# Optimization experiments

Measured on AMD Instinct MI355X. Metric: run time of the kernel, lower is better.

## Reference

```python
import jax, jax.numpy as jnp
import numpy as np

B, N, C, H, E = 16, 512, 128, 8, 131072
Nn = B * N
Dh = C // H
EPS = 1e-5


def setup_inputs() -> dict:
    key = jax.random.key(0)
    ks = jax.random.split(key, 16)
    s = C ** -0.5
    x = jax.random.normal(ks[0], (Nn, C), dtype=jnp.float32)
    edge_index = jax.random.randint(ks[1], (2, E), 0, Nn)
    batch = jnp.arange(Nn) // N  # B equal-sized graphs, sorted
    attn_bias = jax.random.normal(ks[2], (B, N, N, H), dtype=jnp.float32)
    return {
        "x": x,
        "edge_index": edge_index,
        "batch": batch,
        "attn_bias": attn_bias,
        "conv_w": jax.random.normal(ks[3], (C, C)) * s,
        "conv_b": jnp.zeros((C,)),
        "wq": jax.random.normal(ks[4], (C, C)) * s,
        "bq": jnp.zeros((C,)),
        "wk": jax.random.normal(ks[5], (C, C)) * s,
        "bk": jnp.zeros((C,)),
        "wv": jax.random.normal(ks[6], (C, C)) * s,
        "bv": jnp.zeros((C,)),
        "wo": jax.random.normal(ks[7], (C, C)) * s,
        "bo": jnp.zeros((C,)),
        "w1": jax.random.normal(ks[8], (C, 2 * C)) * s,
        "b1": jnp.zeros((2 * C,)),
        "w2": jax.random.normal(ks[9], (2 * C, C)) * (2 * C) ** -0.5,
        "b2": jnp.zeros((C,)),
        "g1": jnp.ones((C,)), "be1": jnp.zeros((C,)),
        "g2": jnp.ones((C,)), "be2": jnp.zeros((C,)),
        "g3": jnp.ones((C,)), "be3": jnp.zeros((C,)),
    }


def _bn(h, g, b):
    # BatchNorm1d over the node dimension (training-mode batch statistics)
    mu = h.mean(axis=0)
    var = h.var(axis=0)  # biased, matches torch normalization
    return g * (h - mu) * jax.lax.rsqrt(var + EPS) + b


def reference(x, edge_index, batch, attn_bias,
              conv_w, conv_b, wq, bq, wk, bk, wv, bv, wo, bo,
              w1, b1, w2, b2, g1, be1, g2, be2, g3, be3):
    n_nodes, ch = x.shape
    bsz, n_max, _, heads = attn_bias.shape
    dh = ch // heads

    # ---- GCN conv (self loops + symmetric norm) -> dropout(0) + residual + norm1
    loops = jnp.arange(n_nodes)
    src = jnp.concatenate([edge_index[0], loops])
    dst = jnp.concatenate([edge_index[1], loops])
    deg = jax.ops.segment_sum(jnp.ones_like(src, dtype=x.dtype), dst, num_segments=n_nodes)
    dinv = jax.lax.rsqrt(jnp.maximum(deg, 1.0))
    xw = x @ conv_w
    msg = xw[src] * (dinv[src] * dinv[dst])[:, None]
    hconv = jax.ops.segment_sum(msg, dst, num_segments=n_nodes) + conv_b
    h1 = _bn(hconv + x, g1, be1)

    # ---- dense batch (equal-sized sorted graphs -> pure reshape, mask all-valid)
    xd = x.reshape(bsz, n_max, ch)
    q = ((xd @ wq + bq) * (dh ** -0.5)).reshape(bsz, n_max, heads, dh)
    k = (xd @ wk + bk).reshape(bsz, n_max, heads, dh)
    v = (xd @ wv + bv).reshape(bsz, n_max, heads, dh)
    scores = jnp.einsum('bqhd,bkhd->bqkh', q, k) + attn_bias  # [B,N,N,H]
    probs = jax.nn.softmax(scores, axis=2)
    att = jnp.einsum('bqkh,bkhd->bqhd', probs, v).reshape(bsz, n_max, ch)
    att = att @ wo + bo
    h2 = _bn(att.reshape(n_nodes, ch) + x, g2, be2)

    # ---- combine branches, MLP with residual, norm3
    out = h1 + h2
    mlp = jax.nn.relu(out @ w1 + b1) @ w2 + b2
    return _bn(out + mlp, g3, be3)
```

## Files before the change

### kernel.cpp

```cpp
#include <hip/hip_runtime.h>
#include <cstddef>

#define NN 8192
#define CC 128

typedef unsigned short u16;
typedef _Float16 half_t;
typedef _Float16 v4h __attribute__((ext_vector_type(4)));
typedef float v4f __attribute__((ext_vector_type(4)));

static __device__ inline u16 f2bf1(float x) {
  unsigned u = __builtin_bit_cast(unsigned, x);
  u += 0x7fffu + ((u >> 16) & 1u);
  return (u16)(u >> 16);
}
static __device__ inline float bf_lo(unsigned u) { return __builtin_bit_cast(float, u << 16); }
static __device__ inline float bf_hi(unsigned u) { return __builtin_bit_cast(float, u & 0xffff0000u); }

typedef __attribute__((address_space(3))) void lvoid_t;
static __device__ inline unsigned lds_addr(void* p) {
  return (unsigned)(unsigned long long)(lvoid_t*)p;
}


__global__ __launch_bounds__(256) void count_deg_int_k(const int* __restrict__ dst, int* degi, int E) {
  int i = blockIdx.x * 256 + threadIdx.x;
  if (i < E) atomicAdd(&degi[dst[i]], 1);
}

__global__ __launch_bounds__(256) void dinv_k(const int* __restrict__ degi, float* __restrict__ dinv, int n) {
  int i = blockIdx.x * 256 + threadIdx.x;
  if (i < n) dinv[i] = rsqrtf((float)(degi[i] + 1));
}

__global__ __launch_bounds__(256) void scan_k(const int* __restrict__ degi, int* __restrict__ rowstart,
                                              int* __restrict__ cursor) {
  __shared__ int partial[256];
  int t = threadIdx.x;
  int base = t * 32;
  int local[32];
  int s = 0;
#pragma unroll
  for (int i = 0; i < 32; ++i) { local[i] = s; s += degi[base + i]; }
  partial[t] = s;
  __syncthreads();
  for (int off = 1; off < 256; off <<= 1) {
    int v = (t >= off) ? partial[t - off] : 0;
    __syncthreads();
    partial[t] += v;
    __syncthreads();
  }
  int offset = partial[t] - s;
#pragma unroll
  for (int i = 0; i < 32; ++i) {
    rowstart[base + i] = offset + local[i];
    cursor[base + i] = offset + local[i];
  }
  if (t == 255) rowstart[NN] = offset + s;
}

__global__ __launch_bounds__(256) void bucket_k(const int* __restrict__ src, const int* __restrict__ dst,
    int* __restrict__ cursor, int* __restrict__ col, int E) {
  int e = blockIdx.x * 256 + threadIdx.x;
  if (e >= E) return;
  int d = dst[e];
  int pos = atomicAdd(&cursor[d], 1);
  col[pos] = src[e];
}

__global__ __launch_bounds__(256) void gather_k(const int* __restrict__ rowstart, const int* __restrict__ col,
    const float* __restrict__ xws, const float* __restrict__ dinv, const float* __restrict__ cb,
    const float* __restrict__ x, float* __restrict__ h1) {
  int d = blockIdx.x * 2 + (threadIdx.x >> 7);
  int c = threadIdx.x & 127;
  int j0 = rowstart[d], j1 = rowstart[d + 1];
  float dd = dinv[d];
  float sum = 0.f;
  float v = 0.f;
  if (j0 < j1) v = xws[(size_t)col[j0] * CC + c];
  for (int j = j0; j < j1; ++j) {
    float v_next = 0.f;
    if (j + 1 < j1) v_next = xws[(size_t)col[j + 1] * CC + c];
    sum += v;
    v = v_next;
  }
  int idx = d * CC + c;
  sum += xws[idx];
  h1[idx] = sum * dd + cb[c] + x[idx];
}


__global__ __launch_bounds__(256) void bn_stats_k(const float* __restrict__ X,
    float* __restrict__ sums, float* __restrict__ sumsq) {
  int t = threadIdx.x;
  int c = t & 127, rg = t >> 7;
  int r0 = blockIdx.x * 64;
  float s = 0.f, sq = 0.f;
  for (int i = 0; i < 32; ++i) {
    float v = X[(size_t)(r0 + rg + 2 * i) * CC + c];
    s += v; sq += v * v;
  }
  atomicAdd(&sums[c], s);
  atomicAdd(&sumsq[c], sq);
}

__global__ __launch_bounds__(256) void combine_k(const float* __restrict__ h1, const float* __restrict__ h2,
    const float* __restrict__ st, const float* __restrict__ g1, const float* __restrict__ be1,
    const float* __restrict__ g2, const float* __restrict__ be2, float* __restrict__ out) {
  int idx = blockIdx.x * 256 + threadIdx.x;
  int c = idx & 127;
  float mu1 = st[c] * (1.f / NN);
  float var1 = st[128 + c] * (1.f / NN) - mu1 * mu1;
  float sc1 = g1[c] * rsqrtf(var1 + 1e-5f);
  float sh1 = be1[c] - mu1 * sc1;
  float mu2 = st[256 + c] * (1.f / NN);
  float var2 = st[384 + c] * (1.f / NN) - mu2 * mu2;
  float sc2 = g2[c] * rsqrtf(var2 + 1e-5f);
  float sh2 = be2[c] - mu2 * sc2;
  out[idx] = sc1 * h1[idx] + sh1 + sc2 * h2[idx] + sh2;
}

__global__ __launch_bounds__(256) void bn_apply_k(const float* __restrict__ h, const float* __restrict__ st,
    const float* __restrict__ g3, const float* __restrict__ be3, float* __restrict__ out) {
  int idx = blockIdx.x * 256 + threadIdx.x;
  int c = idx & 127;
  float mu = st[512 + c] * (1.f / NN);
  float var = st[640 + c] * (1.f / NN) - mu * mu;
  float sc = g3[c] * rsqrtf(var + 1e-5f);
  float sh = be3[c] - mu * sc;
  out[idx] = sc * h[idx] + sh;
}

__global__ __launch_bounds__(256) void gemm_k(const float* __restrict__ A, const float* __restrict__ W,
    const float* __restrict__ bias, const float* __restrict__ resid, const float* __restrict__ dscale,
    float* __restrict__ out, int M, int N, int K, float scale, int relu, int ofp16) {
  __shared__ float As[64 * 132];
  __shared__ float Ws[128 * 64];
  int t = threadIdx.x;
  int ty = t >> 4, tx = t & 15;
  int row0 = blockIdx.x * 64, n0 = blockIdx.y * 64;
  float acc[4][4] = {};
  for (int kc = 0; kc < K; kc += 128) {
#pragma unroll
    for (int j = 0; j < 8; ++j) {
      int f = t + 256 * j;
      int r = f >> 5, c4 = f & 31;
      *(float4*)(As + r * 132 + c4 * 4) = *(const float4*)(A + (size_t)(row0 + r) * K + kc + c4 * 4);
    }
#pragma unroll
    for (int j = 0; j < 8; ++j) {
      int f = t + 256 * j;
      int kr = f >> 4, c4 = f & 15;
      *(float4*)(Ws + kr * 64 + c4 * 4) = *(const float4*)(W + (size_t)(kc + kr) * N + n0 + c4 * 4);
    }
    __syncthreads();
    for (int k0 = 0; k0 < 128; k0 += 4) {
      float a[4][4], b[4][4];
#pragma unroll
      for (int i = 0; i < 4; ++i) {
        float4 t4 = *(const float4*)(As + (4 * ty + i) * 132 + k0);
        a[i][0] = t4.x; a[i][1] = t4.y; a[i][2] = t4.z; a[i][3] = t4.w;
      }
#pragma unroll
      for (int kk = 0; kk < 4; ++kk) {
        float4 t4 = *(const float4*)(Ws + (k0 + kk) * 64 + 4 * tx);
        b[kk][0] = t4.x; b[kk][1] = t4.y; b[kk][2] = t4.z; b[kk][3] = t4.w;
      }
#pragma unroll
      for (int kk = 0; kk < 4; ++kk)
#pragma unroll
        for (int i = 0; i < 4; ++i)
#pragma unroll
          for (int j = 0; j < 4; ++j)
            acc[i][j] += a[i][kk] * b[kk][j];
    }
    __syncthreads();
  }
  float4 bv = make_float4(0.f, 0.f, 0.f, 0.f);
  if (bias) bv = *(const float4*)(bias + n0 + 4 * tx);
#pragma unroll
  for (int i = 0; i < 4; ++i) {
    int row = row0 + 4 * ty + i;
    float ds = dscale ? dscale[row] : 1.f;
    float4 r;
    r.x = (acc[i][0] + bv.x) * scale * ds;
    r.y = (acc[i][1] + bv.y) * scale * ds;
    r.z = (acc[i][2] + bv.z) * scale * ds;
    r.w = (acc[i][3] + bv.w) * scale * ds;
    if (relu) { r.x = fmaxf(r.x, 0.f); r.y = fmaxf(r.y, 0.f); r.z = fmaxf(r.z, 0.f); r.w = fmaxf(r.w, 0.f); }
    size_t o = (size_t)row * N + n0 + 4 * tx;
    if (ofp16) {
      half_t* oh = (half_t*)out;
      v4h hv;
      hv[0] = (half_t)r.x; hv[1] = (half_t)r.y; hv[2] = (half_t)r.z; hv[3] = (half_t)r.w;
      *(v4h*)(oh + o) = hv;
    } else {
      if (resid) {
        float4 rv = *(const float4*)(resid + o);
        r.x += rv.x; r.y += rv.y; r.z += rv.z; r.w += rv.w;
      }
      *(float4*)(out + o) = r;
    }
  }
}

__global__ __launch_bounds__(64, 3) void attn_k(const half_t* __restrict__ Qh,
    const half_t* __restrict__ Kh, const half_t* __restrict__ Vh, const float* __restrict__ bias,
    u16* __restrict__ p0, u16* __restrict__ p1, u16* __restrict__ p2, u16* __restrict__ p3,
    float* __restrict__ lbuf) {
  __shared__ u16 VL[2][2048];
  const int t = threadIdx.x;
  const int orig = blockIdx.x;
  const int s = orig & 7;
  const int qtg = orig >> 3;
  const int b = qtg >> 5;
  const int key0 = s * 64;
  const int node_t = qtg * 16;
  const int kb0 = b * 512 + key0;
  const int lq = t & 15;
  const int lg = t >> 4;

  v4h qf[8];
#pragma unroll
  for (int hd = 0; hd < 8; ++hd)
    qf[hd] = *(const v4h*)(Qh + (size_t)(node_t + lq) * CC + hd * 16 + lg * 4);

  v4f oacc[8];
  float lacc[8];
#pragma unroll
  for (int hd = 0; hd < 8; ++hd) { oacc[hd] = (v4f){0.f, 0.f, 0.f, 0.f}; lacc[hd] = 0.f; }

  const int v_hdb = t >> 5;
  const int v_kg = (t >> 3) & 3;
  const int v_km = (t >> 1) & 3;
  const int v_dm0 = (t & 1) * 8;
  uint4 vreg[4];

  auto vload = [&](int ch) {
#pragma unroll
    for (int i = 0; i < 4; ++i)
      vreg[i] = *(const uint4*)(Vh + (size_t)(kb0 + ch * 16 + v_kg * 4 + v_km) * CC
                                + (i * 2 + v_hdb) * 16 + v_dm0);
  };
  auto vwrite = [&](int bf) {
#pragma unroll
    for (int i = 0; i < 4; ++i)
      *(uint4*)&VL[bf][i * 512 + t * 8] = vreg[i];
  };

  const unsigned lbase = lds_addr(&VL[0][0]);
  const float* bb = bias + ((size_t)node_t * 512 + key0) * 8 + (size_t)lq * 4096;

  vload(0);
  vwrite(0);

  for (int ch = 0; ch < 4; ++ch) {
    const int bf = ch & 1;
    if (ch < 3) vload(ch + 1);

    v4h kf[8];
#pragma unroll
    for (int hd = 0; hd < 8; ++hd)
      kf[hd] = *(const v4h*)(Kh + (size_t)(kb0 + ch * 16 + lq) * CC + hd * 16 + lg * 4);

    asm volatile("s_waitcnt lgkmcnt(0)" ::: "memory");
    __builtin_amdgcn_sched_barrier(0);
    unsigned va = lbase + (unsigned)(bf * 4096) + (unsigned)(t * 8);
    unsigned long long vfr[8];
#pragma unroll
    for (int hd = 0; hd < 8; ++hd)
      asm volatile("ds_read_b64_tr_b16 %0, %1 offset:%2"
                   : "=v"(vfr[hd]) : "v"(va), "i"(hd * 512));
    asm volatile("s_waitcnt lgkmcnt(0)" ::: "memory");
    __builtin_amdgcn_sched_barrier(0);

    if (ch < 3) vwrite(bf ^ 1);

    const v4f z = (v4f){0.f, 0.f, 0.f, 0.f};
#pragma unroll
    for (int hg = 0; hg < 2; ++hg) {
      v4f bfr[4];
#pragma unroll
      for (int reg = 0; reg < 4; ++reg)
        bfr[reg] = *(const v4f*)(bb + (size_t)(ch * 16 + lg * 4 + reg) * 8 + hg * 4);

      v4f stv[4];
#pragma unroll
      for (int j = 0; j < 4; ++j)
        stv[j] = __builtin_amdgcn_mfma_f32_16x16x16f16(kf[hg * 4 + j], qf[hg * 4 + j], z, 0, 0, 0);

#pragma unroll
      for (int j = 0; j < 4; ++j) {
        const int hd = hg * 4 + j;
        float pr0 = __expf(stv[j][0] + bfr[0][j] - 4.f);
        float pr1 = __expf(stv[j][1] + bfr[1][j] - 4.f);
        float pr2 = __expf(stv[j][2] + bfr[2][j] - 4.f);
        float pr3 = __expf(stv[j][3] + bfr[3][j] - 4.f);
        lacc[hd] += pr0 + pr1 + pr2 + pr3;
        unsigned u0 = __builtin_bit_cast(unsigned, __builtin_amdgcn_cvt_pkrtz(pr0, pr1));
        unsigned u1 = __builtin_bit_cast(unsigned, __builtin_amdgcn_cvt_pkrtz(pr2, pr3));
        uint2 pu = make_uint2(u0, u1);
        v4h pa = __builtin_bit_cast(v4h, pu);
        v4h vf = __builtin_bit_cast(v4h, vfr[hd]);
        oacc[hd] = __builtin_amdgcn_mfma_f32_16x16x16f16(pa, vf, oacc[hd], 0, 0, 0);
      }
    }
  }

  u16* preg = (s < 4) ? ((s < 2) ? p0 : p1) : ((s < 6) ? p2 : p3);
  u16* pbase = preg + (size_t)(s & 1) * ((size_t)NN * CC);
#pragma unroll
  for (int hd = 0; hd < 8; ++hd)
#pragma unroll
    for (int reg = 0; reg < 4; ++reg)
      pbase[(((size_t)qtg * 8 + hd) * 4 + reg) * 64 + t] = f2bf1(oacc[hd][reg]);

#pragma unroll
  for (int hd = 0; hd < 8; ++hd) {
    float v = lacc[hd];
    v += __shfl_xor(v, 16);
    v += __shfl_xor(v, 32);
    lacc[hd] = v;
  }
  if (t < 16) {
#pragma unroll
    for (int hd = 0; hd < 8; ++hd)
      lbuf[s * 65536 + (node_t + t) * 8 + hd] = lacc[hd];
  }
}

__global__ __launch_bounds__(256) void attn_merge_k(const u16* __restrict__ p0,
    const u16* __restrict__ p1, const u16* __restrict__ p2, const u16* __restrict__ p3,
    const float* __restrict__ lbuf, float* __restrict__ out) {
  int i = blockIdx.x * 256 + threadIdx.x;
  int node = i >> 3, h = i & 7;
  int tile = node >> 4, q = node & 15;
  float L = 0.f;
#pragma unroll
  for (int s = 0; s < 8; ++s) L += lbuf[s * 65536 + i];
  float inv = 1.f / L;
  float o[16];
#pragma unroll
  for (int d = 0; d < 16; ++d) o[d] = 0.f;
  const u16* regs[4] = {p0, p1, p2, p3};
  size_t base = (((size_t)tile * 8 + h) * 4 + (q & 3)) * 64 + (q >> 2) * 16;
#pragma unroll
  for (int s = 0; s < 8; ++s) {
    const u16* pb = regs[s >> 1] + (size_t)(s & 1) * ((size_t)NN * CC) + base;
    uint4 a = *(const uint4*)pb;
    uint4 b = *(const uint4*)(pb + 8);
    unsigned u[8] = {a.x, a.y, a.z, a.w, b.x, b.y, b.z, b.w};
#pragma unroll
    for (int j = 0; j < 8; ++j) {
      o[2 * j]     += bf_lo(u[j]);
      o[2 * j + 1] += bf_hi(u[j]);
    }
  }
  float* po = out + (size_t)i * 16;
#pragma unroll
  for (int j = 0; j < 4; ++j)
    *(float4*)(po + 4 * j) = make_float4(o[4*j] * inv, o[4*j+1] * inv, o[4*j+2] * inv, o[4*j+3] * inv);
}


extern "C" void kernel_launch(void* const* d_in, const int* in_sizes, int n_in,
                              void* d_out, int out_size, void* d_ws, size_t ws_size,
                              hipStream_t stream) {
  const float* x      = (const float*)d_in[0];
  const int*   ei     = (const int*)d_in[1];
  const float* bias   = (const float*)d_in[3];
  const float* conv_w = (const float*)d_in[4];
  const float* conv_b = (const float*)d_in[5];
  const float* wq = (const float*)d_in[6];
  const float* bq = (const float*)d_in[7];
  const float* wk = (const float*)d_in[8];
  const float* bk = (const float*)d_in[9];
  const float* wv = (const float*)d_in[10];
  const float* bv = (const float*)d_in[11];
  const float* wo = (const float*)d_in[12];
  const float* bo = (const float*)d_in[13];
  const float* w1 = (const float*)d_in[14];
  const float* b1 = (const float*)d_in[15];
  const float* w2 = (const float*)d_in[16];
  const float* b2 = (const float*)d_in[17];
  const float* g1 = (const float*)d_in[18];
  const float* be1 = (const float*)d_in[19];
  const float* g2 = (const float*)d_in[20];
  const float* be2 = (const float*)d_in[21];
  const float* g3 = (const float*)d_in[22];
  const float* be3 = (const float*)d_in[23];
  int E = in_sizes[1] / 2;

  float* ws = (float*)d_ws;
  const size_t NC = (size_t)NN * CC;
  float* xw     = ws;
  float* h1pre  = ws + NC;
  float* qb     = ws + 2 * NC;
  float* kb     = ws + 3 * NC;
  float* vb     = ws + 4 * NC;
  float* h2pre  = ws + 5 * NC;
  float* outbuf = ws + 6 * NC;
  float* hid    = ws + 2 * NC;
  float* h3pre  = ws + 4 * NC;
  float* st     = ws + 7 * NC;
  float* dinv   = ws + 7 * NC + 768;
  int*   degi     = (int*)(ws + 7 * NC + 768 + NN);
  int*   rowstart = degi + NN;
  int*   cursor   = rowstart + NN + 1;
  int*   col      = cursor + NN;
  float* lbuf     = (float*)(col + E);

  hipMemsetAsync(degi, 0, NN * sizeof(int), stream);
  hipMemsetAsync(st, 0, 768 * sizeof(float), stream);

  count_deg_int_k<<<(E + 255) / 256, 256, 0, stream>>>(ei + E, degi, E);
  dinv_k<<<NN / 256, 256, 0, stream>>>(degi, dinv, NN);
  scan_k<<<1, 256, 0, stream>>>(degi, rowstart, cursor);
  bucket_k<<<(E + 255) / 256, 256, 0, stream>>>(ei, ei + E, cursor, col, E);
  gemm_k<<<dim3(NN / 64, 2), 256, 0, stream>>>(x, conv_w, nullptr, nullptr, dinv, xw, NN, CC, CC, 1.f, 0, 0);
  gather_k<<<NN / 2, 256, 0, stream>>>(rowstart, col, xw, dinv, conv_b, x, h1pre);
  bn_stats_k<<<NN / 64, 256, 0, stream>>>(h1pre, st + 0, st + 128);

  gemm_k<<<dim3(NN / 64, 2), 256, 0, stream>>>(x, wq, bq, nullptr, nullptr, qb, NN, CC, CC, 0.25f, 0, 1);
  gemm_k<<<dim3(NN / 64, 2), 256, 0, stream>>>(x, wk, bk, nullptr, nullptr, kb, NN, CC, CC, 1.f, 0, 1);
  gemm_k<<<dim3(NN / 64, 2), 256, 0, stream>>>(x, wv, bv, nullptr, nullptr, vb, NN, CC, CC, 1.f, 0, 1);
  attn_k<<<4096, 64, 0, stream>>>((const half_t*)qb, (const half_t*)kb, (const half_t*)vb, bias,
      (u16*)xw, (u16*)h2pre, (u16*)d_out, (u16*)outbuf, lbuf);
  attn_merge_k<<<65536 / 256, 256, 0, stream>>>((const u16*)xw, (const u16*)h2pre,
      (const u16*)d_out, (const u16*)outbuf, lbuf, vb);
  gemm_k<<<dim3(NN / 64, 2), 256, 0, stream>>>(vb, wo, bo, x, nullptr, h2pre, NN, CC, CC, 1.f, 0, 0);
  bn_stats_k<<<NN / 64, 256, 0, stream>>>(h2pre, st + 256, st + 384);

  combine_k<<<NC / 256, 256, 0, stream>>>(h1pre, h2pre, st, g1, be1, g2, be2, outbuf);
  gemm_k<<<dim3(NN / 64, 4), 256, 0, stream>>>(outbuf, w1, b1, nullptr, nullptr, hid, NN, 2 * CC, CC, 1.f, 1, 0);
  gemm_k<<<dim3(NN / 64, 2), 256, 0, stream>>>(hid, w2, b2, outbuf, nullptr, h3pre, NN, CC, 2 * CC, 1.f, 0, 0);
  bn_stats_k<<<NN / 64, 256, 0, stream>>>(h3pre, st + 512, st + 640);
  bn_apply_k<<<NC / 256, 256, 0, stream>>>(h3pre, st, g3, be3, (float*)d_out);
}
```

Measured before the change: 422.7 us.

## Replace FP32 SIMT GEMM with fp16 MFMA matrix-core GEMM

Swaps the scalar FP32 register-tiled GEMM used for every dense projection (conv, Q/K/V, output, MLP) for an MFMA 16x16x16 fp16 kernel. The weight tile is transposed into LDS as fp16, and A rows are loaded straight from global memory and converted to fp16 in registers. The aim is to move the projection FLOPs off the vector ALUs and onto the matrix cores. The cost is reduced precision on all GEMM inputs (fp16 operands, fp32 accumulation) and narrower, less coalesced scalar output stores.

```diff
diff --git a/kernel.cpp b/kernel.cpp
--- a/kernel.cpp
+++ b/kernel.cpp
@@ -131,75 +131,64 @@
   out[idx] = sc * h[idx] + sh;
 }
 
-__global__ __launch_bounds__(256) void gemm_k(const float* __restrict__ A, const float* __restrict__ W,
+template <int KT>
+__global__ __launch_bounds__(256) void mgemm_k(const float* __restrict__ A, const float* __restrict__ W,
     const float* __restrict__ bias, const float* __restrict__ resid, const float* __restrict__ dscale,
-    float* __restrict__ out, int M, int N, int K, float scale, int relu, int ofp16) {
-  __shared__ float As[64 * 132];
-  __shared__ float Ws[128 * 64];
-  int t = threadIdx.x;
-  int ty = t >> 4, tx = t & 15;
-  int row0 = blockIdx.x * 64, n0 = blockIdx.y * 64;
-  float acc[4][4] = {};
-  for (int kc = 0; kc < K; kc += 128) {
-#pragma unroll
-    for (int j = 0; j < 8; ++j) {
-      int f = t + 256 * j;
-      int r = f >> 5, c4 = f & 31;
-      *(float4*)(As + r * 132 + c4 * 4) = *(const float4*)(A + (size_t)(row0 + r) * K + kc + c4 * 4);
+    float* __restrict__ out, int N, float scale, int relu, int ofp16) {
+  __shared__ half_t Wt[64][KT + 8];
+  const int t = threadIdx.x;
+  const int row0 = blockIdx.x * 64, n0 = blockIdx.y * 64;
+
+#pragma unroll
+  for (int i = 0; i < KT / 4; ++i) {
+    int idx = t + 256 * i;
+    int n = idx & 63, k = idx >> 6;
+    Wt[n][k] = (half_t)W[(size_t)k * N + n0 + n];
+  }
+  __syncthreads();
+
+  const int wv = t >> 6, lg = (t >> 4) & 3, lq = t & 15;
+  const int arow = row0 + wv * 16 + lq;
+
+  v4f af[KT / 16];
+#pragma unroll
+  for (int i = 0; i < KT / 16; ++i)
+    af[i] = *(const v4f*)(A + (size_t)arow * KT + i * 16 + lg * 4);
+
+  v4f acc[4];
+#pragma unroll
+  for (int c = 0; c < 4; ++c) acc[c] = (v4f){0.f, 0.f, 0.f, 0.f};
+
+#pragma unroll
+  for (int i = 0; i < KT / 16; ++i) {
+    v4h a;
+    a[0] = (half_t)af[i][0]; a[1] = (half_t)af[i][1];
+    a[2] = (half_t)af[i][2]; a[3] = (half_t)af[i][3];
+#pragma unroll
+    for (int c = 0; c < 4; ++c) {
+      v4h b = *(const v4h*)&Wt[c * 16 + lq][i * 16 + lg * 4];
+      acc[c] = __builtin_amdgcn_mfma_f32_16x16x16f16(a, b, acc[c], 0, 0, 0);
     }
-#pragma unroll
-    for (int j = 0; j < 8; ++j) {
-      int f = t + 256 * j;
-      int kr = f >> 4, c4 = f & 15;
-      *(float4*)(Ws + kr * 64 + c4 * 4) = *(const float4*)(W + (size_t)(kc + kr) * N + n0 + c4 * 4);
-    }
-    __syncthreads();
-    for (int k0 = 0; k0 < 128; k0 += 4) {
-      float a[4][4], b[4][4];
-#pragma unroll
-      for (int i = 0; i < 4; ++i) {
-        float4 t4 = *(const float4*)(As + (4 * ty + i) * 132 + k0);
-        a[i][0] = t4.x; a[i][1] = t4.y; a[i][2] = t4.z; a[i][3] = t4.w;
+  }
+
+  float bc[4];
+#pragma unroll
+  for (int c = 0; c < 4; ++c) bc[c] = bias ? bias[n0 + c * 16 + lq] : 0.f;
+#pragma unroll
+  for (int reg = 0; reg < 4; ++reg) {
+    int row = row0 + wv * 16 + lg * 4 + reg;
+    float ds = dscale ? dscale[row] : 1.f;
+#pragma unroll
+    for (int c = 0; c < 4; ++c) {
+      float r = (acc[c][reg] + bc[c]) * scale * ds;
+      if (relu) r = fmaxf(r, 0.f);
+      size_t o = (size_t)row * N + n0 + c * 16 + lq;
+      if (ofp16) {
+        ((half_t*)out)[o] = (half_t)r;
+      } else {
+        if (resid) r += resid[o];
+        out[o] = r;
       }
-#pragma unroll
-      for (int kk = 0; kk < 4; ++kk) {
-        float4 t4 = *(const float4*)(Ws + (k0 + kk) * 64 + 4 * tx);
-        b[kk][0] = t4.x; b[kk][1] = t4.y; b[kk][2] = t4.z; b[kk][3] = t4.w;
-      }
-#pragma unroll
-      for (int kk = 0; kk < 4; ++kk)
-#pragma unroll
-        for (int i = 0; i < 4; ++i)
-#pragma unroll
-          for (int j = 0; j < 4; ++j)
-            acc[i][j] += a[i][kk] * b[kk][j];
-    }
-    __syncthreads();
-  }
-  float4 bv = make_float4(0.f, 0.f, 0.f, 0.f);
-  if (bias) bv = *(const float4*)(bias + n0 + 4 * tx);
-#pragma unroll
-  for (int i = 0; i < 4; ++i) {
-    int row = row0 + 4 * ty + i;
-    float ds = dscale ? dscale[row] : 1.f;
-    float4 r;
-    r.x = (acc[i][0] + bv.x) * scale * ds;
-    r.y = (acc[i][1] + bv.y) * scale * ds;
-    r.z = (acc[i][2] + bv.z) * scale * ds;
-    r.w = (acc[i][3] + bv.w) * scale * ds;
-    if (relu) { r.x = fmaxf(r.x, 0.f); r.y = fmaxf(r.y, 0.f); r.z = fmaxf(r.z, 0.f); r.w = fmaxf(r.w, 0.f); }
-    size_t o = (size_t)row * N + n0 + 4 * tx;
-    if (ofp16) {
-      half_t* oh = (half_t*)out;
-      v4h hv;
-      hv[0] = (half_t)r.x; hv[1] = (half_t)r.y; hv[2] = (half_t)r.z; hv[3] = (half_t)r.w;
-      *(v4h*)(oh + o) = hv;
-    } else {
-      if (resid) {
-        float4 rv = *(const float4*)(resid + o);
-        r.x += rv.x; r.y += rv.y; r.z += rv.z; r.w += rv.w;
-      }
-      *(float4*)(out + o) = r;
     }
   }
 }
@@ -417,23 +406,23 @@
   dinv_k<<<NN / 256, 256, 0, stream>>>(degi, dinv, NN);
   scan_k<<<1, 256, 0, stream>>>(degi, rowstart, cursor);
   bucket_k<<<(E + 255) / 256, 256, 0, stream>>>(ei, ei + E, cursor, col, E);
-  gemm_k<<<dim3(NN / 64, 2), 256, 0, stream>>>(x, conv_w, nullptr, nullptr, dinv, xw, NN, CC, CC, 1.f, 0, 0);
+  mgemm_k<128><<<dim3(NN / 64, 2), 256, 0, stream>>>(x, conv_w, nullptr, nullptr, dinv, xw, CC, 1.f, 0, 0);
   gather_k<<<NN / 2, 256, 0, stream>>>(rowstart, col, xw, dinv, conv_b, x, h1pre);
   bn_stats_k<<<NN / 64, 256, 0, stream>>>(h1pre, st + 0, st + 128);
 
-  gemm_k<<<dim3(NN / 64, 2), 256, 0, stream>>>(x, wq, bq, nullptr, nullptr, qb, NN, CC, CC, 0.25f, 0, 1);
-  gemm_k<<<dim3(NN / 64, 2), 256, 0, stream>>>(x, wk, bk, nullptr, nullptr, kb, NN, CC, CC, 1.f, 0, 1);
-  gemm_k<<<dim3(NN / 64, 2), 256, 0, stream>>>(x, wv, bv, nullptr, nullptr, vb, NN, CC, CC, 1.f, 0, 1);
+  mgemm_k<128><<<dim3(NN / 64, 2), 256, 0, stream>>>(x, wq, bq, nullptr, nullptr, qb, CC, 0.25f, 0, 1);
+  mgemm_k<128><<<dim3(NN / 64, 2), 256, 0, stream>>>(x, wk, bk, nullptr, nullptr, kb, CC, 1.f, 0, 1);
+  mgemm_k<128><<<dim3(NN / 64, 2), 256, 0, stream>>>(x, wv, bv, nullptr, nullptr, vb, CC, 1.f, 0, 1);
   attn_k<<<4096, 64, 0, stream>>>((const half_t*)qb, (const half_t*)kb, (const half_t*)vb, bias,
       (u16*)xw, (u16*)h2pre, (u16*)d_out, (u16*)outbuf, lbuf);
   attn_merge_k<<<65536 / 256, 256, 0, stream>>>((const u16*)xw, (const u16*)h2pre,
       (const u16*)d_out, (const u16*)outbuf, lbuf, vb);
-  gemm_k<<<dim3(NN / 64, 2), 256, 0, stream>>>(vb, wo, bo, x, nullptr, h2pre, NN, CC, CC, 1.f, 0, 0);
+  mgemm_k<128><<<dim3(NN / 64, 2), 256, 0, stream>>>(vb, wo, bo, x, nullptr, h2pre, CC, 1.f, 0, 0);
   bn_stats_k<<<NN / 64, 256, 0, stream>>>(h2pre, st + 256, st + 384);
 
   combine_k<<<NC / 256, 256, 0, stream>>>(h1pre, h2pre, st, g1, be1, g2, be2, outbuf);
-  gemm_k<<<dim3(NN / 64, 4), 256, 0, stream>>>(outbuf, w1, b1, nullptr, nullptr, hid, NN, 2 * CC, CC, 1.f, 1, 0);
-  gemm_k<<<dim3(NN / 64, 2), 256, 0, stream>>>(hid, w2, b2, outbuf, nullptr, h3pre, NN, CC, 2 * CC, 1.f, 0, 0);
+  mgemm_k<128><<<dim3(NN / 64, 4), 256, 0, stream>>>(outbuf, w1, b1, nullptr, nullptr, hid, 2 * CC, 1.f, 1, 0);
+  mgemm_k<256><<<dim3(NN / 64, 2), 256, 0, stream>>>(hid, w2, b2, outbuf, nullptr, h3pre, CC, 1.f, 0, 0);
   bn_stats_k<<<NN / 64, 256, 0, stream>>>(h3pre, st + 512, st + 640);
   bn_apply_k<<<NC / 256, 256, 0, stream>>>(h3pre, st, g3, be3, (float*)d_out);
 }
```

After: 467.4 us. 10.6% more time.

## Merge attention key-split partials in LDS within one block, dropping merge kernel

Applied to the files above, without the earlier changes.

The attention kernel now runs one 256-thread block per 16-query tile, with four waves each covering 128 keys instead of eight separate 64-thread blocks per tile. Partial outputs and row sums are reduced through shared memory and normalized in-kernel, so the bf16 partial buffers, their global round trip, and the separate attn_merge launch are gone. In exchange there are only 512 blocks instead of 4096, which cuts parallelism and latency hiding. The LDS footprint also grows, and each wave runs a longer serial loop over its keys.

```diff
diff --git a/kernel.cpp b/kernel.cpp
--- a/kernel.cpp
+++ b/kernel.cpp
@@ -8,14 +8,6 @@
 typedef _Float16 half_t;
 typedef _Float16 v4h __attribute__((ext_vector_type(4)));
 typedef float v4f __attribute__((ext_vector_type(4)));
-
-static __device__ inline u16 f2bf1(float x) {
-  unsigned u = __builtin_bit_cast(unsigned, x);
-  u += 0x7fffu + ((u >> 16) & 1u);
-  return (u16)(u >> 16);
-}
-static __device__ inline float bf_lo(unsigned u) { return __builtin_bit_cast(float, u << 16); }
-static __device__ inline float bf_hi(unsigned u) { return __builtin_bit_cast(float, u & 0xffff0000u); }
 
 typedef __attribute__((address_space(3))) void lvoid_t;
 static __device__ inline unsigned lds_addr(void* p) {
@@ -204,21 +196,21 @@
   }
 }
 
-__global__ __launch_bounds__(64, 3) void attn_k(const half_t* __restrict__ Qh,
+__global__ __launch_bounds__(256, 2) void attn_k(const half_t* __restrict__ Qh,
     const half_t* __restrict__ Kh, const half_t* __restrict__ Vh, const float* __restrict__ bias,
-    u16* __restrict__ p0, u16* __restrict__ p1, u16* __restrict__ p2, u16* __restrict__ p3,
-    float* __restrict__ lbuf) {
-  __shared__ u16 VL[2][2048];
+    float* __restrict__ out) {
+  __shared__ u16 VL[4][2][2048];
+  __shared__ float LB[4][8][16];
   const int t = threadIdx.x;
-  const int orig = blockIdx.x;
-  const int s = orig & 7;
-  const int qtg = orig >> 3;
+  const int wv = t >> 6;
+  const int l = t & 63;
+  const int qtg = blockIdx.x;
   const int b = qtg >> 5;
-  const int key0 = s * 64;
   const int node_t = qtg * 16;
+  const int key0 = wv * 128;
   const int kb0 = b * 512 + key0;
-  const int lq = t & 15;
-  const int lg = t >> 4;
+  const int lq = l & 15;
+  const int lg = l >> 4;
 
   v4h qf[8];
 #pragma unroll
@@ -230,10 +222,10 @@
 #pragma unroll
   for (int hd = 0; hd < 8; ++hd) { oacc[hd] = (v4f){0.f, 0.f, 0.f, 0.f}; lacc[hd] = 0.f; }
 
-  const int v_hdb = t >> 5;
-  const int v_kg = (t >> 3) & 3;
-  const int v_km = (t >> 1) & 3;
-  const int v_dm0 = (t & 1) * 8;
+  const int v_hdb = l >> 5;
+  const int v_kg = (l >> 3) & 3;
+  const int v_km = (l >> 1) & 3;
+  const int v_dm0 = (l & 1) * 8;
   uint4 vreg[4];
 
   auto vload = [&](int ch) {
@@ -245,18 +237,18 @@
   auto vwrite = [&](int bf) {
 #pragma unroll
     for (int i = 0; i < 4; ++i)
-      *(uint4*)&VL[bf][i * 512 + t * 8] = vreg[i];
+      *(uint4*)&VL[wv][bf][i * 512 + l * 8] = vreg[i];
   };
 
-  const unsigned lbase = lds_addr(&VL[0][0]);
+  const unsigned lbase = lds_addr(&VL[wv][0][0]);
   const float* bb = bias + ((size_t)node_t * 512 + key0) * 8 + (size_t)lq * 4096;
 
   vload(0);
   vwrite(0);
 
-  for (int ch = 0; ch < 4; ++ch) {
+  for (int ch = 0; ch < 8; ++ch) {
     const int bf = ch & 1;
-    if (ch < 3) vload(ch + 1);
+    if (ch < 7) vload(ch + 1);
 
     v4h kf[8];
 #pragma unroll
@@ -265,7 +257,7 @@
 
     asm volatile("s_waitcnt lgkmcnt(0)" ::: "memory");
     __builtin_amdgcn_sched_barrier(0);
-    unsigned va = lbase + (unsigned)(bf * 4096) + (unsigned)(t * 8);
+    unsigned va = lbase + (unsigned)(bf * 4096) + (unsigned)(l * 8);
     unsigned long long vfr[8];
 #pragma unroll
     for (int hd = 0; hd < 8; ++hd)
@@ -274,7 +266,7 @@
     asm volatile("s_waitcnt lgkmcnt(0)" ::: "memory");
     __builtin_amdgcn_sched_barrier(0);
 
-    if (ch < 3) vwrite(bf ^ 1);
+    if (ch < 7) vwrite(bf ^ 1);
 
     const v4f z = (v4f){0.f, 0.f, 0.f, 0.f};
 #pragma unroll
@@ -307,14 +299,6 @@
     }
   }
 
-  u16* preg = (s < 4) ? ((s < 2) ? p0 : p1) : ((s < 6) ? p2 : p3);
-  u16* pbase = preg + (size_t)(s & 1) * ((size_t)NN * CC);
-#pragma unroll
-  for (int hd = 0; hd < 8; ++hd)
-#pragma unroll
-    for (int reg = 0; reg < 4; ++reg)
-      pbase[(((size_t)qtg * 8 + hd) * 4 + reg) * 64 + t] = f2bf1(oacc[hd][reg]);
-
 #pragma unroll
   for (int hd = 0; hd < 8; ++hd) {
     float v = lacc[hd];
@@ -322,44 +306,34 @@
     v += __shfl_xor(v, 32);
     lacc[hd] = v;
   }
-  if (t < 16) {
+  if (l < 16) {
 #pragma unroll
     for (int hd = 0; hd < 8; ++hd)
-      lbuf[s * 65536 + (node_t + t) * 8 + hd] = lacc[hd];
-  }
-}
-
-__global__ __launch_bounds__(256) void attn_merge_k(const u16* __restrict__ p0,
-    const u16* __restrict__ p1, const u16* __restrict__ p2, const u16* __restrict__ p3,
-    const float* __restrict__ lbuf, float* __restrict__ out) {
-  int i = blockIdx.x * 256 + threadIdx.x;
-  int node = i >> 3, h = i & 7;
-  int tile = node >> 4, q = node & 15;
-  float L = 0.f;
-#pragma unroll
-  for (int s = 0; s < 8; ++s) L += lbuf[s * 65536 + i];
-  float inv = 1.f / L;
-  float o[16];
-#pragma unroll
-  for (int d = 0; d < 16; ++d) o[d] = 0.f;
-  const u16* regs[4] = {p0, p1, p2, p3};
-  size_t base = (((size_t)tile * 8 + h) * 4 + (q & 3)) * 64 + (q >> 2) * 16;
-#pragma unroll
-  for (int s = 0; s < 8; ++s) {
-    const u16* pb = regs[s >> 1] + (size_t)(s & 1) * ((size_t)NN * CC) + base;
-    uint4 a = *(const uint4*)pb;
-    uint4 b = *(const uint4*)(pb + 8);
-    unsigned u[8] = {a.x, a.y, a.z, a.w, b.x, b.y, b.z, b.w};
-#pragma unroll
-    for (int j = 0; j < 8; ++j) {
-      o[2 * j]     += bf_lo(u[j]);
-      o[2 * j + 1] += bf_hi(u[j]);
-    }
-  }
-  float* po = out + (size_t)i * 16;
-#pragma unroll
-  for (int j = 0; j < 4; ++j)
-    *(float4*)(po + 4 * j) = make_float4(o[4*j] * inv, o[4*j+1] * inv, o[4*j+2] * inv, o[4*j+3] * inv);
+      LB[wv][hd][l] = lacc[hd];
+  }
+
+  float* FB = (float*)VL;
+#pragma unroll
+  for (int hd = 0; hd < 8; ++hd)
+#pragma unroll
+    for (int reg = 0; reg < 4; ++reg)
+      FB[wv * 2048 + (lg * 4 + reg) * 128 + hd * 16 + lq] = oacc[hd][reg];
+
+  __syncthreads();
+
+  const int q = t >> 4, d0 = (t & 15) * 8;
+  float res[8];
+#pragma unroll
+  for (int j = 0; j < 8; ++j) {
+    int d = d0 + j, hd = d >> 4;
+    float v = FB[q * 128 + d] + FB[2048 + q * 128 + d]
+            + FB[4096 + q * 128 + d] + FB[6144 + q * 128 + d];
+    float L = LB[0][hd][q] + LB[1][hd][q] + LB[2][hd][q] + LB[3][hd][q];
+    res[j] = v / L;
+  }
+  float* po = out + (size_t)(node_t + q) * CC + d0;
+  *(float4*)po       = make_float4(res[0], res[1], res[2], res[3]);
+  *(float4*)(po + 4) = make_float4(res[4], res[5], res[6], res[7]);
 }
 
 
@@ -408,7 +382,6 @@
   int*   rowstart = degi + NN;
   int*   cursor   = rowstart + NN + 1;
   int*   col      = cursor + NN;
-  float* lbuf     = (float*)(col + E);
 
   hipMemsetAsync(degi, 0, NN * sizeof(int), stream);
   hipMemsetAsync(st, 0, 768 * sizeof(float), stream);
@@ -424,11 +397,8 @@
   gemm_k<<<dim3(NN / 64, 2), 256, 0, stream>>>(x, wq, bq, nullptr, nullptr, qb, NN, CC, CC, 0.25f, 0, 1);
   gemm_k<<<dim3(NN / 64, 2), 256, 0, stream>>>(x, wk, bk, nullptr, nullptr, kb, NN, CC, CC, 1.f, 0, 1);
   gemm_k<<<dim3(NN / 64, 2), 256, 0, stream>>>(x, wv, bv, nullptr, nullptr, vb, NN, CC, CC, 1.f, 0, 1);
-  attn_k<<<4096, 64, 0, stream>>>((const half_t*)qb, (const half_t*)kb, (const half_t*)vb, bias,
-      (u16*)xw, (u16*)h2pre, (u16*)d_out, (u16*)outbuf, lbuf);
-  attn_merge_k<<<65536 / 256, 256, 0, stream>>>((const u16*)xw, (const u16*)h2pre,
-      (const u16*)d_out, (const u16*)outbuf, lbuf, vb);
-  gemm_k<<<dim3(NN / 64, 2), 256, 0, stream>>>(vb, wo, bo, x, nullptr, h2pre, NN, CC, CC, 1.f, 0, 0);
+  attn_k<<<512, 256, 0, stream>>>((const half_t*)qb, (const half_t*)kb, (const half_t*)vb, bias, outbuf);
+  gemm_k<<<dim3(NN / 64, 2), 256, 0, stream>>>(outbuf, wo, bo, x, nullptr, h2pre, NN, CC, CC, 1.f, 0, 0);
   bn_stats_k<<<NN / 64, 256, 0, stream>>>(h2pre, st + 256, st + 384);
 
   combine_k<<<NC / 256, 256, 0, stream>>>(h1pre, h2pre, st, g1, be1, g2, be2, outbuf);
```

After: 413.9 us. 2.1% less time.
